# Performance work log

Measured on AMD Instinct MI355X. Metric: run time of the kernel, lower is better.

The kernel has to match this reference:

```python
import jax, jax.numpy as jnp
import numpy as np

N_NODES = 50000


def gcn_conv(x, W, b, src, dst, n_nodes):
    # PyG GCNConv: h = D^{-1/2}(A+I)D^{-1/2} X W + b, with self-loops added.
    h = x @ W                                   # [N, H]
    loops = jnp.arange(n_nodes, dtype=src.dtype)
    s = jnp.concatenate([src, loops])           # [E+N]
    d = jnp.concatenate([dst, loops])
    deg = jax.ops.segment_sum(jnp.ones_like(d, dtype=h.dtype), d, num_segments=n_nodes)
    dinv = jnp.where(deg > 0, jax.lax.rsqrt(deg), 0.0)
    norm = dinv[s] * dinv[d]                    # [E+N]
    msg = h[s] * norm[:, None]                  # gather + scale
    agg = jax.ops.segment_sum(msg, d, num_segments=n_nodes)  # scatter-add
    return agg + b


def setup_inputs() -> dict:
    key = jax.random.key(0)
    ks = jax.random.split(key, 8)
    N, E, D, H, ED = N_NODES, 800000, 64, 64, 16
    sc = lambda f_in: 1.0 / np.sqrt(f_in)
    return {
        "x": jax.random.normal(ks[0], (N, D), dtype=jnp.float32),
        "src": jax.random.randint(ks[1], (E,), 0, N),
        "dst": jax.random.randint(ks[2], (E,), 0, N),
        "edge_attr": jax.random.normal(ks[3], (E, ED), dtype=jnp.float32),
        "W1": jax.random.normal(ks[4], (D, H), dtype=jnp.float32) * sc(D),
        "b1": jnp.zeros((H,), dtype=jnp.float32),
        "Wm1": jax.random.normal(ks[5], (2 * H + ED, H), dtype=jnp.float32) * sc(2 * H + ED),
        "bm1": jnp.zeros((H,), dtype=jnp.float32),
        "Wm2": jax.random.normal(ks[6], (H, 1), dtype=jnp.float32) * sc(H),
        "bm2": jnp.zeros((1,), dtype=jnp.float32),
    }


def reference(x, src, dst, edge_attr, W1, b1, Wm1, bm1, Wm2, bm2):
    h = jax.nn.relu(gcn_conv(x, W1, b1, src, dst, N_NODES))  # [N, H]
    edge_repr = jnp.concatenate([h[src], h[dst], edge_attr], axis=1)  # [E, 2H+ED]
    hidden = jax.nn.relu(edge_repr @ Wm1 + bm1)
    scores = jax.nn.sigmoid(hidden @ Wm2 + bm2)
    return scores.squeeze(-1)
```

## Files before the change

kernel.cpp:

```cpp
#include <hip/hip_runtime.h>
#include <math.h>


typedef __attribute__((ext_vector_type(8))) short bf16x8;
typedef __attribute__((ext_vector_type(4))) float f32x4;

#define MAXDEG 64
#define BSHIFT 7
#define BMASK 127
#define NBUCK 391
#define CAP 2560
#define CHUNK 4096
#define BINB 196
#define GEMB 782
#define BPB 40

__device__ __forceinline__ unsigned short f2b(float f) {
    unsigned u = __float_as_uint(f);
    unsigned r = (u + 0x7FFFu + ((u >> 16) & 1u)) >> 16;
    return (unsigned short)r;
}

__global__ void __launch_bounds__(256) bin_gemm_pack(
        const int* __restrict__ dst, const int* __restrict__ src,
        unsigned int* __restrict__ region, int* __restrict__ gcur, int E,
        const float* __restrict__ x, const float* __restrict__ W1,
        unsigned short* __restrict__ gbf,
        const float* __restrict__ Wm1, unsigned short* __restrict__ Bp, int N) {
    __shared__ __align__(16) char smem[32768];
    const int bid = blockIdx.x, tid = threadIdx.x;

    if (bid < BINB) {
        int* lc = (int*)smem;
        int* s0 = lc + 512;
        int* s1 = s0 + 512;
        int* gb = s1 + 512;
        unsigned* lval = (unsigned*)(gb + 512);
        unsigned short* lbuk = (unsigned short*)(lval + 4096);

        for (int i = tid; i < 512; i += 256) lc[i] = 0;
        __syncthreads();

        unsigned kb[16], kv[16];
#pragma unroll
        for (int j = 0; j < 4; ++j) {
            int i4 = bid * 1024 + j * 256 + tid;
            bool ok = (i4 * 4 < E);
            int4 d4 = make_int4(0, 0, 0, 0), s4 = make_int4(0, 0, 0, 0);
            if (ok) { d4 = ((const int4*)dst)[i4]; s4 = ((const int4*)src)[i4]; }
            int dd[4] = {d4.x, d4.y, d4.z, d4.w};
            int ss[4] = {s4.x, s4.y, s4.z, s4.w};
#pragma unroll
            for (int k = 0; k < 4; ++k) {
                int idx = j * 4 + k;
                kb[idx] = 0xFFFFFFFFu;
                if (ok) {
                    int b = dd[k] >> BSHIFT;
                    int r = atomicAdd(&lc[b], 1);
                    kb[idx] = ((unsigned)b << 12) | (unsigned)r;
                    kv[idx] = ((unsigned)(dd[k] & BMASK) << 16) | (unsigned)ss[k];
                }
            }
        }
        __syncthreads();

        for (int i = tid; i < 512; i += 256) s0[i] = lc[i];
        __syncthreads();
        int* pin = s0; int* pout = s1;
        for (int off = 1; off < 512; off <<= 1) {
            for (int i = tid; i < 512; i += 256) {
                int v = pin[i];
                if (i >= off) v += pin[i - off];
                pout[i] = v;
            }
            __syncthreads();
            int* t = pin; pin = pout; pout = t;
        }
        int* lb = pout;
        for (int i = tid; i < 512; i += 256) lb[i] = pin[i] - lc[i];
        for (int i = tid; i < NBUCK; i += 256) {
            int c = lc[i];
            gb[i] = c ? atomicAdd(&gcur[i], c) : 0;
        }
        __syncthreads();

#pragma unroll
        for (int idx = 0; idx < 16; ++idx) {
            if (kb[idx] != 0xFFFFFFFFu) {
                int b = (int)(kb[idx] >> 12), r = (int)(kb[idx] & 4095u);
                int pos = lb[b] + r;
                lval[pos] = kv[idx];
                lbuk[pos] = (unsigned short)b;
            }
        }
        __syncthreads();

        int ne = E - bid * CHUNK; if (ne > CHUNK) ne = CHUNK;
        for (int i = tid; i < ne; i += 256) {
            int b = lbuk[i];
            int idx = gb[b] + (i - lb[b]);
            if (idx < CAP) region[(size_t)b * CAP + idx] = lval[i];
        }
    } else if (bid < BINB + GEMB) {
        unsigned short* sB = (unsigned short*)smem;
        for (int i = tid; i < 4096; i += 256) {
            int j = i & 7, ln = (i >> 3) & 63, t = (i >> 9) & 3, s = i >> 11;
            int k = s * 32 + (ln >> 4) * 8 + j, col = t * 16 + (ln & 15);
            sB[i] = f2b(W1[k * 64 + col]);
        }
        __syncthreads();
        int wid = (bid - BINB) * 4 + (tid >> 6);
        int NWT = N / 16;
        if (wid < NWT) {
            int lane = tid & 63, m = lane & 15, quad = lane >> 4;
            int r0 = wid * 16;
            f32x4 acc[4];
#pragma unroll
            for (int t = 0; t < 4; ++t) acc[t] = (f32x4){0.f, 0.f, 0.f, 0.f};
            const bf16x8* bp = (const bf16x8*)sB;
#pragma unroll
            for (int s = 0; s < 2; ++s) {
                const float4* xp = (const float4*)(x + (size_t)(r0 + m) * 64 + s * 32 + quad * 8);
                float4 v0 = xp[0], v1 = xp[1];
                bf16x8 a;
                a[0] = (short)f2b(v0.x); a[1] = (short)f2b(v0.y);
                a[2] = (short)f2b(v0.z); a[3] = (short)f2b(v0.w);
                a[4] = (short)f2b(v1.x); a[5] = (short)f2b(v1.y);
                a[6] = (short)f2b(v1.z); a[7] = (short)f2b(v1.w);
#pragma unroll
                for (int t = 0; t < 4; ++t)
                    acc[t] = __builtin_amdgcn_mfma_f32_16x16x32_bf16(
                        a, bp[(s * 4 + t) * 64 + lane], acc[t], 0, 0, 0);
            }
#pragma unroll
            for (int reg = 0; reg < 4; ++reg) {
                int row = r0 + quad * 4 + reg;
#pragma unroll
                for (int t = 0; t < 4; ++t)
                    gbf[(size_t)row * 64 + t * 16 + m] = f2b(acc[t][reg]);
            }
        }
    } else {
        int idx = (bid - BINB - GEMB) * 256 + tid;
        if (idx < 10240) {
            int j = idx & 7, ln = (idx >> 3) & 63, t = (idx >> 9) & 3, s = idx >> 11;
            int k = s * 32 + (ln >> 4) * 8 + j, col = t * 16 + (ln & 15);
            float v = (k < 144) ? Wm1[k * 64 + col] : 0.0f;
            Bp[idx] = f2b(v);
        }
    }
}

__global__ void __launch_bounds__(256) build_csr(
        const unsigned int* __restrict__ region, const int* __restrict__ gcur,
        int* __restrict__ cnt, unsigned short* __restrict__ csr_pad, int N) {
    __shared__ unsigned short lcsr[128 * MAXDEG];
    __shared__ int lcnt[128];
    int b = blockIdx.x, tid = threadIdx.x;
    if (tid < 128) lcnt[tid] = 0;
    __syncthreads();
    int ecnt = gcur[b]; if (ecnt > CAP) ecnt = CAP;
    const unsigned int* reg = region + (size_t)b * CAP;
    for (int i = tid; i < ecnt; i += 256) {
        unsigned v = reg[i];
        int dloc = (int)(v >> 16), s = (int)(v & 0xFFFFu);
        int r = atomicAdd(&lcnt[dloc], 1);
        if (r < MAXDEG) lcsr[dloc * MAXDEG + r] = (unsigned short)s;
    }
    __syncthreads();
    int n0 = b << BSHIFT;
    int nb = N - n0; if (nb > 128) nb = 128;
    if (tid < nb) cnt[n0 + tid] = lcnt[tid];
    int4* gout = (int4*)(csr_pad + (size_t)n0 * MAXDEG);
    const int4* lin = (const int4*)lcsr;
    int tot = nb * 8;
    for (int i = tid; i < tot; i += 256) gout[i] = lin[i];
}

__global__ void __launch_bounds__(256) gather_finalize(
        const unsigned short* __restrict__ gbf, const unsigned short* __restrict__ csr_pad,
        const int* __restrict__ cnt, const float* __restrict__ b1,
        unsigned short* __restrict__ hbf, int N) {
    int wid = blockIdx.x * 4 + (threadIdx.x >> 6);
    if (wid >= N) return;
    int lane = threadIdx.x & 63;
    int n8 = lane >> 3, c8 = lane & 7;
    int deg = cnt[wid];
    if (deg > MAXDEG) deg = MAXDEG;
    size_t base = (size_t)wid << 6;
    const int4* gb4 = (const int4*)gbf;
    float a[8];
#pragma unroll
    for (int k = 0; k < 8; ++k) a[k] = 0.f;

    for (int j0 = 0; j0 < deg; j0 += 64) {
        int nidx = j0 + lane;
        int sidx = 0; float dsv = 0.f;
        if (nidx < deg) {
            sidx = (int)csr_pad[base + nidx];
            dsv = rsqrtf((float)cnt[sidx] + 1.0f);
        }
        int c = deg - j0; if (c > 64) c = 64;
        for (int step = 0; step * 8 < c; ++step) {
            int nn = step * 8 + n8;
            int srow = __shfl(sidx, nn, 64);
            float ds = __shfl(dsv, nn, 64);
            int4 u = make_int4(0, 0, 0, 0);
            if (nn < c) u = gb4[(size_t)srow * 8 + c8];
            a[0] += ds * __uint_as_float((unsigned)u.x << 16);
            a[1] += ds * __uint_as_float((unsigned)u.x & 0xffff0000u);
            a[2] += ds * __uint_as_float((unsigned)u.y << 16);
            a[3] += ds * __uint_as_float((unsigned)u.y & 0xffff0000u);
            a[4] += ds * __uint_as_float((unsigned)u.z << 16);
            a[5] += ds * __uint_as_float((unsigned)u.z & 0xffff0000u);
            a[6] += ds * __uint_as_float((unsigned)u.w << 16);
            a[7] += ds * __uint_as_float((unsigned)u.w & 0xffff0000u);
        }
    }
#pragma unroll
    for (int mask = 8; mask < 64; mask <<= 1) {
#pragma unroll
        for (int k = 0; k < 8; ++k) a[k] += __shfl_xor(a[k], mask, 64);
    }
    float dd = rsqrtf((float)deg + 1.0f);
    {
        int4 u = gb4[(size_t)wid * 8 + c8];
        a[0] += dd * __uint_as_float((unsigned)u.x << 16);
        a[1] += dd * __uint_as_float((unsigned)u.x & 0xffff0000u);
        a[2] += dd * __uint_as_float((unsigned)u.y << 16);
        a[3] += dd * __uint_as_float((unsigned)u.y & 0xffff0000u);
        a[4] += dd * __uint_as_float((unsigned)u.z << 16);
        a[5] += dd * __uint_as_float((unsigned)u.z & 0xffff0000u);
        a[6] += dd * __uint_as_float((unsigned)u.w << 16);
        a[7] += dd * __uint_as_float((unsigned)u.w & 0xffff0000u);
    }
    if (n8 == 0) {
        const float4* bv = (const float4*)(b1 + c8 * 8);
        float4 b0 = bv[0], b14 = bv[1];
        float h0 = dd * a[0] + b0.x,  h1 = dd * a[1] + b0.y;
        float h2 = dd * a[2] + b0.z,  h3 = dd * a[3] + b0.w;
        float h4 = dd * a[4] + b14.x, h5 = dd * a[5] + b14.y;
        float h6 = dd * a[6] + b14.z, h7 = dd * a[7] + b14.w;
        h0 = h0 > 0.f ? h0 : 0.f; h1 = h1 > 0.f ? h1 : 0.f;
        h2 = h2 > 0.f ? h2 : 0.f; h3 = h3 > 0.f ? h3 : 0.f;
        h4 = h4 > 0.f ? h4 : 0.f; h5 = h5 > 0.f ? h5 : 0.f;
        h6 = h6 > 0.f ? h6 : 0.f; h7 = h7 > 0.f ? h7 : 0.f;
        int4 w;
        w.x = (int)((unsigned)f2b(h0) | ((unsigned)f2b(h1) << 16));
        w.y = (int)((unsigned)f2b(h2) | ((unsigned)f2b(h3) << 16));
        w.z = (int)((unsigned)f2b(h4) | ((unsigned)f2b(h5) << 16));
        w.w = (int)((unsigned)f2b(h6) | ((unsigned)f2b(h7) << 16));
        ((int4*)hbf)[(size_t)wid * 8 + c8] = w;
    }
}

__global__ void __launch_bounds__(256, 8) edge_mlp_mfma(
        const unsigned short* __restrict__ hbf, const float* __restrict__ ea,
        const int* __restrict__ src, const int* __restrict__ dst,
        const unsigned short* __restrict__ Bp,
        const float* __restrict__ bm1, const float* __restrict__ Wm2,
        const float* __restrict__ bm2, float* __restrict__ out, int E) {
    __shared__ unsigned short sB[10240];
    {
        const int4* gB = (const int4*)Bp;
        int4* lB = (int4*)sB;
#pragma unroll
        for (int i = 0; i < 5; ++i)
            lB[threadIdx.x + i * 256] = gB[threadIdx.x + i * 256];
    }
    __syncthreads();
    int lane = threadIdx.x & 63;
    int wave = threadIdx.x >> 6;
    int m = lane & 15, quad = lane >> 4;
    int e0 = (blockIdx.x * 4 + wave) * 16;
    if (e0 >= E) return;
    int e = e0 + m;
    int ec = e < E ? e : E - 1;
    int si = src[ec], di = dst[ec];
    bf16x8 af[5];
    af[0] = *(const bf16x8*)(hbf + (size_t)si * 64 + quad * 8);
    af[1] = *(const bf16x8*)(hbf + (size_t)si * 64 + 32 + quad * 8);
    af[2] = *(const bf16x8*)(hbf + (size_t)di * 64 + quad * 8);
    af[3] = *(const bf16x8*)(hbf + (size_t)di * 64 + 32 + quad * 8);
    if (quad < 2) {
        const float4* ep = (const float4*)(ea + (size_t)ec * 16 + quad * 8);
        float4 v0 = ep[0], v1 = ep[1];
        af[4][0] = (short)f2b(v0.x); af[4][1] = (short)f2b(v0.y);
        af[4][2] = (short)f2b(v0.z); af[4][3] = (short)f2b(v0.w);
        af[4][4] = (short)f2b(v1.x); af[4][5] = (short)f2b(v1.y);
        af[4][6] = (short)f2b(v1.z); af[4][7] = (short)f2b(v1.w);
    } else {
#pragma unroll
        for (int j = 0; j < 8; ++j) af[4][j] = 0;
    }
    __builtin_amdgcn_sched_barrier(0);
    f32x4 acc[4];
#pragma unroll
    for (int t = 0; t < 4; ++t) acc[t] = (f32x4){0.f, 0.f, 0.f, 0.f};
    const bf16x8* bp = (const bf16x8*)sB;
#pragma unroll
    for (int s = 0; s < 5; ++s) {
#pragma unroll
        for (int t = 0; t < 4; ++t)
            acc[t] = __builtin_amdgcn_mfma_f32_16x16x32_bf16(
                af[s], bp[(s * 4 + t) * 64 + lane], acc[t], 0, 0, 0);
    }
    float w2[4], bb[4];
#pragma unroll
    for (int t = 0; t < 4; ++t) {
        int col = t * 16 + m;
        bb[t] = bm1[col];
        w2[t] = Wm2[col];
    }
    float pr[4];
#pragma unroll
    for (int r = 0; r < 4; ++r) {
        float sum = 0.0f;
#pragma unroll
        for (int t = 0; t < 4; ++t) {
            float hv = acc[t][r] + bb[t];
            sum += (hv > 0.0f ? hv : 0.0f) * w2[t];
        }
        pr[r] = sum;
    }
#pragma unroll
    for (int off = 1; off < 16; off <<= 1) {
#pragma unroll
        for (int r = 0; r < 4; ++r) pr[r] += __shfl_xor(pr[r], off, 64);
    }
    float b2 = bm2[0];
    if (m < 4) {
        int eo = e0 + quad * 4 + m;
        if (eo < E) out[eo] = 1.0f / (1.0f + __expf(-(pr[m] + b2)));
    }
}

extern "C" void kernel_launch(void* const* d_in, const int* in_sizes, int n_in,
                              void* d_out, int out_size, void* d_ws, size_t ws_size,
                              hipStream_t stream) {
    const float* x   = (const float*)d_in[0];
    const int*   src = (const int*)d_in[1];
    const int*   dst = (const int*)d_in[2];
    const float* ea  = (const float*)d_in[3];
    const float* W1  = (const float*)d_in[4];
    const float* b1  = (const float*)d_in[5];
    const float* Wm1 = (const float*)d_in[6];
    const float* bm1 = (const float*)d_in[7];
    const float* Wm2 = (const float*)d_in[8];
    const float* bm2 = (const float*)d_in[9];
    float* out = (float*)d_out;

    int N = in_sizes[0] / 64;
    int E = in_sizes[1];

    char* p = (char*)d_ws;
    unsigned short* gbf     = (unsigned short*)p; p += (size_t)N * 64 * 2;
    unsigned short* hbf     = (unsigned short*)p; p += (size_t)N * 64 * 2;
    unsigned short* csr_pad = (unsigned short*)p; p += (size_t)N * MAXDEG * 2;
    int*            cnt     = (int*)p;            p += (size_t)N * 4;
    int*            gcur    = (int*)p;            p += (size_t)((NBUCK * 4 + 15) / 16) * 16;
    unsigned short* Bp      = (unsigned short*)p; p += 10240 * 2;
    unsigned int*   region  = (unsigned int*)hbf;

    hipMemsetAsync(gcur, 0, NBUCK * sizeof(int), stream);
    bin_gemm_pack<<<BINB + GEMB + BPB, 256, 0, stream>>>(
        dst, src, region, gcur, E, x, W1, gbf, Wm1, Bp, N);
    build_csr<<<NBUCK, 256, 0, stream>>>(region, gcur, cnt, csr_pad, N);
    gather_finalize<<<(N + 3) / 4, 256, 0, stream>>>(gbf, csr_pad, cnt, b1, hbf, N);
    edge_mlp_mfma<<<(E + 63) / 64, 256, 0, stream>>>(hbf, ea, src, dst, Bp,
                                                     bm1, Wm2, bm2, out, E);
}
```

Measured before the change: 190.7 us.

## Pre-scale node GEMM rows by source degree norm and use 8-thread-per-node gather

Moves the X·W1 GEMM out of the fused binning kernel into its own kernel that runs after CSR construction, so each output row can be multiplied by its source-side rsqrt(deg+1) before storage. The gather kernel then only sums neighbor rows, with no per-edge degree lookup or multiply, and is restructured from one wave per node with shuffles and a cross-lane reduction to 8 threads per node with a 4-way unrolled neighbor loop. This removes the per-edge cnt gathers, shuffles and the final xor reduction. In exchange it adds a kernel launch, serializes the GEMM after binning where it previously overlapped, and rounds the pre-scaled values to bf16.

```diff
diff --git a/kernel.cpp b/kernel.cpp
--- a/kernel.cpp
+++ b/kernel.cpp
@@ -12,7 +12,6 @@
 #define CAP 2560
 #define CHUNK 4096
 #define BINB 196
-#define GEMB 782
 #define BPB 40
 
 __device__ __forceinline__ unsigned short f2b(float f) {
@@ -21,12 +20,10 @@
     return (unsigned short)r;
 }
 
-__global__ void __launch_bounds__(256) bin_gemm_pack(
+__global__ void __launch_bounds__(256) bin_pack(
         const int* __restrict__ dst, const int* __restrict__ src,
         unsigned int* __restrict__ region, int* __restrict__ gcur, int E,
-        const float* __restrict__ x, const float* __restrict__ W1,
-        unsigned short* __restrict__ gbf,
-        const float* __restrict__ Wm1, unsigned short* __restrict__ Bp, int N) {
+        const float* __restrict__ Wm1, unsigned short* __restrict__ Bp) {
     __shared__ __align__(16) char smem[32768];
     const int bid = blockIdx.x, tid = threadIdx.x;
 
@@ -101,47 +98,8 @@
             int idx = gb[b] + (i - lb[b]);
             if (idx < CAP) region[(size_t)b * CAP + idx] = lval[i];
         }
-    } else if (bid < BINB + GEMB) {
-        unsigned short* sB = (unsigned short*)smem;
-        for (int i = tid; i < 4096; i += 256) {
-            int j = i & 7, ln = (i >> 3) & 63, t = (i >> 9) & 3, s = i >> 11;
-            int k = s * 32 + (ln >> 4) * 8 + j, col = t * 16 + (ln & 15);
-            sB[i] = f2b(W1[k * 64 + col]);
-        }
-        __syncthreads();
-        int wid = (bid - BINB) * 4 + (tid >> 6);
-        int NWT = N / 16;
-        if (wid < NWT) {
-            int lane = tid & 63, m = lane & 15, quad = lane >> 4;
-            int r0 = wid * 16;
-            f32x4 acc[4];
-#pragma unroll
-            for (int t = 0; t < 4; ++t) acc[t] = (f32x4){0.f, 0.f, 0.f, 0.f};
-            const bf16x8* bp = (const bf16x8*)sB;
-#pragma unroll
-            for (int s = 0; s < 2; ++s) {
-                const float4* xp = (const float4*)(x + (size_t)(r0 + m) * 64 + s * 32 + quad * 8);
-                float4 v0 = xp[0], v1 = xp[1];
-                bf16x8 a;
-                a[0] = (short)f2b(v0.x); a[1] = (short)f2b(v0.y);
-                a[2] = (short)f2b(v0.z); a[3] = (short)f2b(v0.w);
-                a[4] = (short)f2b(v1.x); a[5] = (short)f2b(v1.y);
-                a[6] = (short)f2b(v1.z); a[7] = (short)f2b(v1.w);
-#pragma unroll
-                for (int t = 0; t < 4; ++t)
-                    acc[t] = __builtin_amdgcn_mfma_f32_16x16x32_bf16(
-                        a, bp[(s * 4 + t) * 64 + lane], acc[t], 0, 0, 0);
-            }
-#pragma unroll
-            for (int reg = 0; reg < 4; ++reg) {
-                int row = r0 + quad * 4 + reg;
-#pragma unroll
-                for (int t = 0; t < 4; ++t)
-                    gbf[(size_t)row * 64 + t * 16 + m] = f2b(acc[t][reg]);
-            }
-        }
     } else {
-        int idx = (bid - BINB - GEMB) * 256 + tid;
+        int idx = (bid - BINB) * 256 + tid;
         if (idx < 10240) {
             int j = idx & 7, ln = (idx >> 3) & 63, t = (idx >> 9) & 3, s = idx >> 11;
             int k = s * 32 + (ln >> 4) * 8 + j, col = t * 16 + (ln & 15);
@@ -177,81 +135,110 @@
     for (int i = tid; i < tot; i += 256) gout[i] = lin[i];
 }
 
+__global__ void __launch_bounds__(256) node_gemm_mfma(
+        const float* __restrict__ x, const float* __restrict__ W1,
+        const int* __restrict__ cnt, unsigned short* __restrict__ gbf, int NWT) {
+    __shared__ unsigned short sB[4096];
+    for (int i = threadIdx.x; i < 4096; i += 256) {
+        int j = i & 7, ln = (i >> 3) & 63, t = (i >> 9) & 3, s = i >> 11;
+        int k = s * 32 + (ln >> 4) * 8 + j, col = t * 16 + (ln & 15);
+        sB[i] = f2b(W1[k * 64 + col]);
+    }
+    __syncthreads();
+    int wid = blockIdx.x * 4 + (threadIdx.x >> 6);
+    if (wid >= NWT) return;
+    int lane = threadIdx.x & 63, m = lane & 15, quad = lane >> 4;
+    int r0 = wid * 16;
+    f32x4 acc[4];
+#pragma unroll
+    for (int t = 0; t < 4; ++t) acc[t] = (f32x4){0.f, 0.f, 0.f, 0.f};
+    const bf16x8* bp = (const bf16x8*)sB;
+#pragma unroll
+    for (int s = 0; s < 2; ++s) {
+        const float4* xp = (const float4*)(x + (size_t)(r0 + m) * 64 + s * 32 + quad * 8);
+        float4 v0 = xp[0], v1 = xp[1];
+        bf16x8 a;
+        a[0] = (short)f2b(v0.x); a[1] = (short)f2b(v0.y);
+        a[2] = (short)f2b(v0.z); a[3] = (short)f2b(v0.w);
+        a[4] = (short)f2b(v1.x); a[5] = (short)f2b(v1.y);
+        a[6] = (short)f2b(v1.z); a[7] = (short)f2b(v1.w);
+#pragma unroll
+        for (int t = 0; t < 4; ++t)
+            acc[t] = __builtin_amdgcn_mfma_f32_16x16x32_bf16(
+                a, bp[(s * 4 + t) * 64 + lane], acc[t], 0, 0, 0);
+    }
+#pragma unroll
+    for (int reg = 0; reg < 4; ++reg) {
+        int row = r0 + quad * 4 + reg;
+        float di = rsqrtf((float)cnt[row] + 1.0f);
+#pragma unroll
+        for (int t = 0; t < 4; ++t)
+            gbf[(size_t)row * 64 + t * 16 + m] = f2b(acc[t][reg] * di);
+    }
+}
+
+#define ACC8(U) \
+    a0 += __uint_as_float((unsigned)(U).x << 16); \
+    a1 += __uint_as_float((unsigned)(U).x & 0xffff0000u); \
+    a2 += __uint_as_float((unsigned)(U).y << 16); \
+    a3 += __uint_as_float((unsigned)(U).y & 0xffff0000u); \
+    a4 += __uint_as_float((unsigned)(U).z << 16); \
+    a5 += __uint_as_float((unsigned)(U).z & 0xffff0000u); \
+    a6 += __uint_as_float((unsigned)(U).w << 16); \
+    a7 += __uint_as_float((unsigned)(U).w & 0xffff0000u);
+
 __global__ void __launch_bounds__(256) gather_finalize(
         const unsigned short* __restrict__ gbf, const unsigned short* __restrict__ csr_pad,
         const int* __restrict__ cnt, const float* __restrict__ b1,
         unsigned short* __restrict__ hbf, int N) {
-    int wid = blockIdx.x * 4 + (threadIdx.x >> 6);
-    if (wid >= N) return;
-    int lane = threadIdx.x & 63;
-    int n8 = lane >> 3, c8 = lane & 7;
-    int deg = cnt[wid];
+    int t = blockIdx.x * 256 + threadIdx.x;
+    int node = t >> 3;
+    if (node >= N) return;
+    int c8 = t & 7;
+    int deg = cnt[node];
     if (deg > MAXDEG) deg = MAXDEG;
-    size_t base = (size_t)wid << 6;
+    size_t base = (size_t)node << 6;
     const int4* gb4 = (const int4*)gbf;
-    float a[8];
-#pragma unroll
-    for (int k = 0; k < 8; ++k) a[k] = 0.f;
-
-    for (int j0 = 0; j0 < deg; j0 += 64) {
-        int nidx = j0 + lane;
-        int sidx = 0; float dsv = 0.f;
-        if (nidx < deg) {
-            sidx = (int)csr_pad[base + nidx];
-            dsv = rsqrtf((float)cnt[sidx] + 1.0f);
-        }
-        int c = deg - j0; if (c > 64) c = 64;
-        for (int step = 0; step * 8 < c; ++step) {
-            int nn = step * 8 + n8;
-            int srow = __shfl(sidx, nn, 64);
-            float ds = __shfl(dsv, nn, 64);
-            int4 u = make_int4(0, 0, 0, 0);
-            if (nn < c) u = gb4[(size_t)srow * 8 + c8];
-            a[0] += ds * __uint_as_float((unsigned)u.x << 16);
-            a[1] += ds * __uint_as_float((unsigned)u.x & 0xffff0000u);
-            a[2] += ds * __uint_as_float((unsigned)u.y << 16);
-            a[3] += ds * __uint_as_float((unsigned)u.y & 0xffff0000u);
-            a[4] += ds * __uint_as_float((unsigned)u.z << 16);
-            a[5] += ds * __uint_as_float((unsigned)u.z & 0xffff0000u);
-            a[6] += ds * __uint_as_float((unsigned)u.w << 16);
-            a[7] += ds * __uint_as_float((unsigned)u.w & 0xffff0000u);
-        }
-    }
-#pragma unroll
-    for (int mask = 8; mask < 64; mask <<= 1) {
-#pragma unroll
-        for (int k = 0; k < 8; ++k) a[k] += __shfl_xor(a[k], mask, 64);
+    float a0 = 0.f, a1 = 0.f, a2 = 0.f, a3 = 0.f,
+          a4 = 0.f, a5 = 0.f, a6 = 0.f, a7 = 0.f;
+    int j = 0;
+    for (; j + 4 <= deg; j += 4) {
+        int s0 = (int)csr_pad[base + j];
+        int s1 = (int)csr_pad[base + j + 1];
+        int s2 = (int)csr_pad[base + j + 2];
+        int s3 = (int)csr_pad[base + j + 3];
+        int4 u0 = gb4[(size_t)s0 * 8 + c8];
+        int4 u1 = gb4[(size_t)s1 * 8 + c8];
+        int4 u2 = gb4[(size_t)s2 * 8 + c8];
+        int4 u3 = gb4[(size_t)s3 * 8 + c8];
+        ACC8(u0) ACC8(u1) ACC8(u2) ACC8(u3)
+    }
+    for (; j < deg; ++j) {
+        int s0 = (int)csr_pad[base + j];
+        int4 u0 = gb4[(size_t)s0 * 8 + c8];
+        ACC8(u0)
+    }
+    {
+        int4 u = gb4[(size_t)node * 8 + c8];
+        ACC8(u)
     }
     float dd = rsqrtf((float)deg + 1.0f);
-    {
-        int4 u = gb4[(size_t)wid * 8 + c8];
-        a[0] += dd * __uint_as_float((unsigned)u.x << 16);
-        a[1] += dd * __uint_as_float((unsigned)u.x & 0xffff0000u);
-        a[2] += dd * __uint_as_float((unsigned)u.y << 16);
-        a[3] += dd * __uint_as_float((unsigned)u.y & 0xffff0000u);
-        a[4] += dd * __uint_as_float((unsigned)u.z << 16);
-        a[5] += dd * __uint_as_float((unsigned)u.z & 0xffff0000u);
-        a[6] += dd * __uint_as_float((unsigned)u.w << 16);
-        a[7] += dd * __uint_as_float((unsigned)u.w & 0xffff0000u);
-    }
-    if (n8 == 0) {
-        const float4* bv = (const float4*)(b1 + c8 * 8);
-        float4 b0 = bv[0], b14 = bv[1];
-        float h0 = dd * a[0] + b0.x,  h1 = dd * a[1] + b0.y;
-        float h2 = dd * a[2] + b0.z,  h3 = dd * a[3] + b0.w;
-        float h4 = dd * a[4] + b14.x, h5 = dd * a[5] + b14.y;
-        float h6 = dd * a[6] + b14.z, h7 = dd * a[7] + b14.w;
-        h0 = h0 > 0.f ? h0 : 0.f; h1 = h1 > 0.f ? h1 : 0.f;
-        h2 = h2 > 0.f ? h2 : 0.f; h3 = h3 > 0.f ? h3 : 0.f;
-        h4 = h4 > 0.f ? h4 : 0.f; h5 = h5 > 0.f ? h5 : 0.f;
-        h6 = h6 > 0.f ? h6 : 0.f; h7 = h7 > 0.f ? h7 : 0.f;
-        int4 w;
-        w.x = (int)((unsigned)f2b(h0) | ((unsigned)f2b(h1) << 16));
-        w.y = (int)((unsigned)f2b(h2) | ((unsigned)f2b(h3) << 16));
-        w.z = (int)((unsigned)f2b(h4) | ((unsigned)f2b(h5) << 16));
-        w.w = (int)((unsigned)f2b(h6) | ((unsigned)f2b(h7) << 16));
-        ((int4*)hbf)[(size_t)wid * 8 + c8] = w;
-    }
+    const float4* bv = (const float4*)(b1 + c8 * 8);
+    float4 b0 = bv[0], b14 = bv[1];
+    float h0 = dd * a0 + b0.x,  h1 = dd * a1 + b0.y;
+    float h2 = dd * a2 + b0.z,  h3 = dd * a3 + b0.w;
+    float h4 = dd * a4 + b14.x, h5 = dd * a5 + b14.y;
+    float h6 = dd * a6 + b14.z, h7 = dd * a7 + b14.w;
+    h0 = h0 > 0.f ? h0 : 0.f; h1 = h1 > 0.f ? h1 : 0.f;
+    h2 = h2 > 0.f ? h2 : 0.f; h3 = h3 > 0.f ? h3 : 0.f;
+    h4 = h4 > 0.f ? h4 : 0.f; h5 = h5 > 0.f ? h5 : 0.f;
+    h6 = h6 > 0.f ? h6 : 0.f; h7 = h7 > 0.f ? h7 : 0.f;
+    int4 w;
+    w.x = (int)((unsigned)f2b(h0) | ((unsigned)f2b(h1) << 16));
+    w.y = (int)((unsigned)f2b(h2) | ((unsigned)f2b(h3) << 16));
+    w.z = (int)((unsigned)f2b(h4) | ((unsigned)f2b(h5) << 16));
+    w.w = (int)((unsigned)f2b(h6) | ((unsigned)f2b(h7) << 16));
+    ((int4*)hbf)[(size_t)node * 8 + c8] = w;
 }
 
 __global__ void __launch_bounds__(256, 8) edge_mlp_mfma(
@@ -352,6 +339,7 @@
 
     int N = in_sizes[0] / 64;
     int E = in_sizes[1];
+    int NWT = N / 16;
 
     char* p = (char*)d_ws;
     unsigned short* gbf     = (unsigned short*)p; p += (size_t)N * 64 * 2;
@@ -363,10 +351,10 @@
     unsigned int*   region  = (unsigned int*)hbf;
 
     hipMemsetAsync(gcur, 0, NBUCK * sizeof(int), stream);
-    bin_gemm_pack<<<BINB + GEMB + BPB, 256, 0, stream>>>(
-        dst, src, region, gcur, E, x, W1, gbf, Wm1, Bp, N);
+    bin_pack<<<BINB + BPB, 256, 0, stream>>>(dst, src, region, gcur, E, Wm1, Bp);
     build_csr<<<NBUCK, 256, 0, stream>>>(region, gcur, cnt, csr_pad, N);
-    gather_finalize<<<(N + 3) / 4, 256, 0, stream>>>(gbf, csr_pad, cnt, b1, hbf, N);
+    node_gemm_mfma<<<(NWT + 3) / 4, 256, 0, stream>>>(x, W1, cnt, gbf, NWT);
+    gather_finalize<<<(N * 8 + 255) / 256, 256, 0, stream>>>(gbf, csr_pad, cnt, b1, hbf, N);
     edge_mlp_mfma<<<(E + 63) / 64, 256, 0, stream>>>(hbf, ea, src, dst, Bp,
                                                      bm1, Wm2, bm2, out, E);
 }
```

After: 189.0 us. Within noise of the previous version (-0.9%).
